# Performance work log

Hardware: AMD Instinct MI355X
Metric: run time of the kernel (lower is better)

The kernel has to match this reference:

```python
import jax, jax.numpy as jnp
import numpy as np

H = 1024      # hidden_size
NH = 4        # n_head
NP = 8        # num_points
PRED = 20     # pred_dim
FF = 4 * H    # dim_feedforward
FEATS = {"m0": 2048, "m1": 1024, "m2": 512}
B = 8192


def _ln(x, g, b, eps=1e-5):
    mu = x.mean(-1, keepdims=True)
    var = ((x - mu) ** 2).mean(-1, keepdims=True)
    return (x - mu) * jax.lax.rsqrt(var + eps) * g + b


def setup_inputs() -> dict:
    key = jax.random.key(0)
    ks = iter(jax.random.split(key, 64))
    d = {}
    d["x_m0"] = jax.random.normal(next(ks), (B, FEATS["m0"]), jnp.float32)
    d["x_m1"] = jax.random.normal(next(ks), (B, 8, FEATS["m1"]), jnp.float32)  # 3D -> mean over dim 1
    d["x_m2"] = jax.random.normal(next(ks), (B, FEATS["m2"]), jnp.float32)

    def p(shape):
        return jax.random.normal(next(ks), shape, jnp.float32) * 0.02

    # modality projectors (Linear stored as [in, out]; y = x @ W + b)
    for mm, f in FEATS.items():
        d[f"Wp_{mm}"] = p((f, H)); d[f"bp_{mm}"] = jnp.zeros((H,), jnp.float32)
    # gated fusion
    d["Wg"] = p((H * 3, 3)); d["bg"] = jnp.zeros((3,), jnp.float32)
    # deformable cross attention
    d["Woff"] = p((H, NH * NP)); d["boff"] = jnp.zeros((NH * NP,), jnp.float32)
    d["Watt"] = p((H, NH * NP)); d["batt"] = jnp.zeros((NH * NP,), jnp.float32)
    d["Wproj"] = p((H * NH, H)); d["bproj"] = jnp.zeros((H,), jnp.float32)
    # FFN + layernorms
    d["W1"] = p((H, FF)); d["b1"] = jnp.zeros((FF,), jnp.float32)
    d["W2"] = p((FF, H)); d["b2"] = jnp.zeros((H,), jnp.float32)
    d["g1"] = jnp.ones((H,), jnp.float32); d["be1"] = jnp.zeros((H,), jnp.float32)
    d["g2"] = jnp.ones((H,), jnp.float32); d["be2"] = jnp.zeros((H,), jnp.float32)
    # head
    d["Wh"] = p((H, PRED)); d["bh"] = jnp.zeros((PRED,), jnp.float32)
    return d


def reference(x_m0, x_m1, x_m2, Wp_m0, bp_m0, Wp_m1, bp_m1, Wp_m2, bp_m2,
              Wg, bg, Woff, boff, Watt, batt, Wproj, bproj,
              W1, b1, W2, b2, g1, be1, g2, be2, Wh, bh):
    # modality projection (dropout is identity in eval mode)
    r0 = jax.nn.relu(x_m0 @ Wp_m0 + bp_m0)
    r1 = jax.nn.relu(x_m1.mean(axis=1) @ Wp_m1 + bp_m1)  # mean over dim 1 for 3D input
    r2 = jax.nn.relu(x_m2 @ Wp_m2 + bp_m2)

    # gated fusion (all modalities present -> mask adds 0 everywhere)
    cat = jnp.concatenate([r0, r1, r2], axis=-1)            # [B, 3H]
    gw = jax.nn.softmax(cat @ Wg + bg, axis=-1)             # [B, 3]
    fused = jnp.einsum('bm,bmh->bh', gw, jnp.stack([r0, r1, r2], axis=1))

    src = fused[:, None, :]                                  # [B, Lq=1, H]
    Bsz, Lq, C = src.shape
    Lk = Lq

    # DeformableCrossAttention(src, src, src)
    off = jax.nn.sigmoid((src @ Woff + boff).reshape(Bsz, Lq, NH, NP)) * (Lk - 1)
    idx = jnp.clip(off.astype(jnp.int32), 0, Lk - 1)         # torch .long() truncation (non-negative)
    al = (src @ Watt + batt).reshape(Bsz, Lq, NH, NP)
    # per-batch gather of key/value rows at sampled indices; key == value == src
    sk = jax.vmap(lambda k, i: k[i])(src, idx)               # [B, Lq, NH, NP, C]
    scores = (src[:, :, None, None, :] * sk).sum(-1) / jnp.sqrt(jnp.float32(C)) + al
    w = jax.nn.softmax(scores, axis=-1)                      # softmax over points
    attn = (w[..., None] * sk).sum(axis=3).reshape(Bsz, Lq, NH * C)
    src2 = attn @ Wproj + bproj

    src = _ln(src + src2, g1, be1)
    src2 = jax.nn.gelu(src @ W1 + b1, approximate=False) @ W2 + b2
    src = _ln(src + src2, g2, be2)

    pooled = src.mean(axis=1)                                # [B, H]
    logits = pooled @ Wh + bh                                # [B, PRED]
    hazards = jax.nn.sigmoid(logits)
    survival = jnp.cumprod(1.0 - hazards, axis=1)
    return hazards, survival
```

## Files before the change

### kernel.cpp

```cpp
#include <hip/hip_runtime.h>
#include <hip/hip_bf16.h>


#define B_ROWS 8192
#define HDIM 1024
#define F0 2048
#define F1 1024
#define F2 512
#define FFDIM 4096
#define NPRED 20

typedef __bf16 bf16x8 __attribute__((ext_vector_type(8)));
typedef float f32x4 __attribute__((ext_vector_type(4)));

__device__ __forceinline__ unsigned short f2bf(float f) {
    unsigned int u = __builtin_bit_cast(unsigned int, f);
    u += 0x7FFFu + ((u >> 16) & 1u);
    return (unsigned short)(u >> 16);
}
__device__ __forceinline__ float bf2f(unsigned short s) {
    unsigned int u = ((unsigned int)s) << 16;
    return __builtin_bit_cast(float, u);
}
__device__ __forceinline__ unsigned int pack2(float lo, float hi) {
    return (unsigned int)f2bf(lo) | ((unsigned int)f2bf(hi) << 16);
}

template <int EPI>
__global__ __launch_bounds__(256) void gemm_bt(
    const unsigned short* __restrict__ A,
    const unsigned short* __restrict__ Bt,
    const float* __restrict__ bias,
    const float* __restrict__ resid,
    void* __restrict__ outp,
    int N, int K)
{
    __shared__ __attribute__((aligned(16))) unsigned short lsA[128 * 64];
    __shared__ __attribute__((aligned(16))) unsigned short lsB[128 * 64];
    const int t = threadIdx.x;
    const int lane = t & 63;
    const int wid = t >> 6;
    const int bn = blockIdx.x, bm = blockIdx.y;
    const int wr = wid >> 1, wc = wid & 1;

    f32x4 acc[4][4] = {};

    int rowj[4], scj[4];
#pragma unroll
    for (int j = 0; j < 4; ++j) {
        int o = j * 4096 + wid * 1024 + lane * 16;
        int r = o >> 7;
        int c16 = (o >> 4) & 7;
        rowj[j] = r;
        scj[j] = c16 ^ (r & 7);
    }
    const unsigned short* Abase = A + (size_t)bm * 128 * K;
    const unsigned short* Bbase = Bt + (size_t)bn * 128 * K;

    const int ktiles = K >> 6;
    for (int kt = 0; kt < ktiles; ++kt) {
        const int k0 = kt * 64;
#pragma unroll
        for (int j = 0; j < 4; ++j) {
            const unsigned short* ga = Abase + (size_t)rowj[j] * K + k0 + scj[j] * 8;
            const unsigned short* gb = Bbase + (size_t)rowj[j] * K + k0 + scj[j] * 8;
            __builtin_amdgcn_global_load_lds(
                (const __attribute__((address_space(1))) unsigned int*)ga,
                (__attribute__((address_space(3))) unsigned int*)(lsA + j * 2048 + wid * 512),
                16, 0, 0);
            __builtin_amdgcn_global_load_lds(
                (const __attribute__((address_space(1))) unsigned int*)gb,
                (__attribute__((address_space(3))) unsigned int*)(lsB + j * 2048 + wid * 512),
                16, 0, 0);
        }
        __syncthreads();
#pragma unroll
        for (int ks = 0; ks < 2; ++ks) {
            bf16x8 af[4], bfr[4];
            const int kc = ks * 4 + (lane >> 4);
#pragma unroll
            for (int m = 0; m < 4; ++m) {
                int r = wr * 64 + m * 16 + (lane & 15);
                af[m] = *(const bf16x8*)(lsA + r * 64 + ((kc ^ (r & 7)) << 3));
            }
#pragma unroll
            for (int n = 0; n < 4; ++n) {
                int r = wc * 64 + n * 16 + (lane & 15);
                bfr[n] = *(const bf16x8*)(lsB + r * 64 + ((kc ^ (r & 7)) << 3));
            }
#pragma unroll
            for (int m = 0; m < 4; ++m)
#pragma unroll
                for (int n = 0; n < 4; ++n)
                    acc[m][n] = __builtin_amdgcn_mfma_f32_16x16x32_bf16(
                        af[m], bfr[n], acc[m][n], 0, 0, 0);
        }
        __syncthreads();
    }

#pragma unroll
    for (int n = 0; n < 4; ++n) {
        const int col = bn * 128 + wc * 64 + n * 16 + (lane & 15);
        const float bv = bias[col];
#pragma unroll
        for (int m = 0; m < 4; ++m) {
            const int row0 = bm * 128 + wr * 64 + m * 16 + ((lane >> 4) << 2);
#pragma unroll
            for (int r2 = 0; r2 < 4; ++r2) {
                const size_t idx = (size_t)(row0 + r2) * N + col;
                float v = acc[m][n][r2] + bv;
                if (EPI == 0) {
                    v = v > 0.f ? v : 0.f;
                    ((unsigned short*)outp)[idx] = f2bf(v);
                } else if (EPI == 1) {
                    float g = 0.5f * v * (1.f + erff(v * 0.70710678118654752f));
                    ((unsigned short*)outp)[idx] = f2bf(g);
                } else {
                    ((float*)outp)[idx] = v + resid[idx];
                }
            }
        }
    }
}

template <int OUT_BF16>
__global__ void transpose_k(const float* __restrict__ in, void* __restrict__ out,
                            int R, int C)
{
    __shared__ float tile[32][33];
    const int r0 = blockIdx.y * 32, c0 = blockIdx.x * 32;
    const int tx = threadIdx.x, ty = threadIdx.y;
#pragma unroll
    for (int i = 0; i < 4; ++i) {
        int r = r0 + ty + i * 8, c = c0 + tx;
        if (r < R && c < C) tile[ty + i * 8][tx] = in[(size_t)r * C + c];
    }
    __syncthreads();
#pragma unroll
    for (int i = 0; i < 4; ++i) {
        int c = c0 + ty + i * 8, r = r0 + tx;
        if (r < R && c < C) {
            float v = tile[tx][ty + i * 8];
            if (OUT_BF16) ((unsigned short*)out)[(size_t)c * R + r] = f2bf(v);
            else          ((float*)out)[(size_t)c * R + r] = v;
        }
    }
}

__global__ void wproj_sum_k(const float* __restrict__ Wproj,
                            unsigned short* __restrict__ WPT)
{
    __shared__ float tile[32][33];
    const int k0 = blockIdx.y * 32, n0 = blockIdx.x * 32;
    const int tx = threadIdx.x, ty = threadIdx.y;
#pragma unroll
    for (int i = 0; i < 4; ++i) {
        int k = k0 + ty + i * 8, n = n0 + tx;
        float s = 0.f;
#pragma unroll
        for (int h = 0; h < 4; ++h) s += Wproj[(size_t)(h * HDIM + k) * HDIM + n];
        tile[ty + i * 8][tx] = s;
    }
    __syncthreads();
#pragma unroll
    for (int i = 0; i < 4; ++i) {
        int n = n0 + ty + i * 8, k = k0 + tx;
        WPT[(size_t)n * HDIM + k] = f2bf(tile[tx][ty + i * 8]);
    }
}

__global__ void cvt_f32_bf16_k(const float* __restrict__ in,
                               unsigned short* __restrict__ out, int n8)
{
    for (int i = blockIdx.x * blockDim.x + threadIdx.x; i < n8;
         i += gridDim.x * blockDim.x) {
        const float4* p = (const float4*)(in + (size_t)i * 8);
        float4 a = p[0], b = p[1];
        uint4 o;
        o.x = pack2(a.x, a.y); o.y = pack2(a.z, a.w);
        o.z = pack2(b.x, b.y); o.w = pack2(b.z, b.w);
        *(uint4*)(out + (size_t)i * 8) = o;
    }
}

__global__ void mean8_k(const float* __restrict__ x, unsigned short* __restrict__ out,
                        int nq)
{
    for (int q = blockIdx.x * blockDim.x + threadIdx.x; q < nq;
         q += gridDim.x * blockDim.x) {
        int b = q >> 8, c4 = (q & 255) << 2;
        const float* base = x + (size_t)b * 8 * HDIM + c4;
        float4 s = {0.f, 0.f, 0.f, 0.f};
#pragma unroll
        for (int s8 = 0; s8 < 8; ++s8) {
            float4 v = *(const float4*)(base + s8 * HDIM);
            s.x += v.x; s.y += v.y; s.z += v.z; s.w += v.w;
        }
        uint2 o;
        o.x = pack2(s.x * 0.125f, s.y * 0.125f);
        o.y = pack2(s.z * 0.125f, s.w * 0.125f);
        *(uint2*)(out + (size_t)b * HDIM + c4) = o;
    }
}

__global__ __launch_bounds__(256) void gating_k(
    const unsigned short* __restrict__ r0p, const unsigned short* __restrict__ r1p,
    const unsigned short* __restrict__ r2p,
    const float* __restrict__ WgT,
    const float* __restrict__ bg,
    unsigned short* __restrict__ fusedb, float* __restrict__ fusedf)
{
    const int row = blockIdx.x * 4 + (threadIdx.x >> 6);
    const int lane = threadIdx.x & 63;
    float rv[3][16];
    const unsigned short* rp[3] = {r0p, r1p, r2p};
#pragma unroll
    for (int m = 0; m < 3; ++m) {
        const uint4* p = (const uint4*)(rp[m] + (size_t)row * HDIM + lane * 16);
        uint4 u0 = p[0], u1 = p[1];
        unsigned int w[8] = {u0.x, u0.y, u0.z, u0.w, u1.x, u1.y, u1.z, u1.w};
#pragma unroll
        for (int q = 0; q < 8; ++q) {
            rv[m][q * 2]     = bf2f((unsigned short)(w[q] & 0xffffu));
            rv[m][q * 2 + 1] = bf2f((unsigned short)(w[q] >> 16));
        }
    }
    float s[3] = {0.f, 0.f, 0.f};
#pragma unroll
    for (int j = 0; j < 3; ++j) {
#pragma unroll
        for (int m = 0; m < 3; ++m) {
            const float* wp = WgT + j * 3072 + m * HDIM + lane * 16;
#pragma unroll
            for (int e = 0; e < 16; ++e) s[j] += rv[m][e] * wp[e];
        }
    }
#pragma unroll
    for (int j = 0; j < 3; ++j)
#pragma unroll
        for (int off = 32; off > 0; off >>= 1) s[j] += __shfl_xor(s[j], off);

    float s0 = s[0] + bg[0], s1 = s[1] + bg[1], s2 = s[2] + bg[2];
    float mx = fmaxf(s0, fmaxf(s1, s2));
    float e0 = expf(s0 - mx), e1 = expf(s1 - mx), e2 = expf(s2 - mx);
    float inv = 1.f / (e0 + e1 + e2);
    float g0 = e0 * inv, g1 = e1 * inv, g2 = e2 * inv;

    float f[16];
#pragma unroll
    for (int e = 0; e < 16; ++e)
        f[e] = g0 * rv[0][e] + g1 * rv[1][e] + g2 * rv[2][e];

    float4* ff = (float4*)(fusedf + (size_t)row * HDIM + lane * 16);
#pragma unroll
    for (int q = 0; q < 4; ++q) {
        float4 v = {f[q * 4], f[q * 4 + 1], f[q * 4 + 2], f[q * 4 + 3]};
        ff[q] = v;
    }
    uint4* fb = (uint4*)(fusedb + (size_t)row * HDIM + lane * 16);
    uint4 o0, o1;
    o0.x = pack2(f[0], f[1]);  o0.y = pack2(f[2], f[3]);
    o0.z = pack2(f[4], f[5]);  o0.w = pack2(f[6], f[7]);
    o1.x = pack2(f[8], f[9]);  o1.y = pack2(f[10], f[11]);
    o1.z = pack2(f[12], f[13]); o1.w = pack2(f[14], f[15]);
    fb[0] = o0; fb[1] = o1;
}

__global__ __launch_bounds__(256) void ln_k(
    const float* __restrict__ z, const float* __restrict__ g,
    const float* __restrict__ be,
    unsigned short* __restrict__ yb, float* __restrict__ yf)
{
    const int row = blockIdx.x * 4 + (threadIdx.x >> 6);
    const int lane = threadIdx.x & 63;
    const float4* zp = (const float4*)(z + (size_t)row * HDIM + lane * 16);
    float x[16];
    float4 v0 = zp[0], v1 = zp[1], v2 = zp[2], v3 = zp[3];
    x[0]=v0.x; x[1]=v0.y; x[2]=v0.z; x[3]=v0.w;
    x[4]=v1.x; x[5]=v1.y; x[6]=v1.z; x[7]=v1.w;
    x[8]=v2.x; x[9]=v2.y; x[10]=v2.z; x[11]=v2.w;
    x[12]=v3.x; x[13]=v3.y; x[14]=v3.z; x[15]=v3.w;
    float sum = 0.f, sq = 0.f;
#pragma unroll
    for (int e = 0; e < 16; ++e) { sum += x[e]; sq += x[e] * x[e]; }
#pragma unroll
    for (int off = 32; off > 0; off >>= 1) {
        sum += __shfl_xor(sum, off);
        sq  += __shfl_xor(sq, off);
    }
    float mu = sum * (1.f / HDIM);
    float var = sq * (1.f / HDIM) - mu * mu;
    float rs = rsqrtf(var + 1e-5f);
    const float4* gp = (const float4*)(g + lane * 16);
    const float4* bp = (const float4*)(be + lane * 16);
    float y[16];
#pragma unroll
    for (int q = 0; q < 4; ++q) {
        float4 gv = gp[q], bv = bp[q];
        y[q*4+0] = (x[q*4+0] - mu) * rs * gv.x + bv.x;
        y[q*4+1] = (x[q*4+1] - mu) * rs * gv.y + bv.y;
        y[q*4+2] = (x[q*4+2] - mu) * rs * gv.z + bv.z;
        y[q*4+3] = (x[q*4+3] - mu) * rs * gv.w + bv.w;
    }
    float4* yfp = (float4*)(yf + (size_t)row * HDIM + lane * 16);
#pragma unroll
    for (int q = 0; q < 4; ++q) {
        float4 v = {y[q*4], y[q*4+1], y[q*4+2], y[q*4+3]};
        yfp[q] = v;
    }
    uint4* ybp = (uint4*)(yb + (size_t)row * HDIM + lane * 16);
    uint4 o0, o1;
    o0.x = pack2(y[0], y[1]);   o0.y = pack2(y[2], y[3]);
    o0.z = pack2(y[4], y[5]);   o0.w = pack2(y[6], y[7]);
    o1.x = pack2(y[8], y[9]);   o1.y = pack2(y[10], y[11]);
    o1.z = pack2(y[12], y[13]); o1.w = pack2(y[14], y[15]);
    ybp[0] = o0; ybp[1] = o1;
}

__global__ __launch_bounds__(256) void head_k(
    const float* __restrict__ z, const float* __restrict__ g,
    const float* __restrict__ be,
    const float* __restrict__ WhT,
    const float* __restrict__ bh, float* __restrict__ out)
{
    const int row = blockIdx.x * 4 + (threadIdx.x >> 6);
    const int lane = threadIdx.x & 63;
    const float4* zp = (const float4*)(z + (size_t)row * HDIM + lane * 16);
    float x[16];
    float4 v0 = zp[0], v1 = zp[1], v2 = zp[2], v3 = zp[3];
    x[0]=v0.x; x[1]=v0.y; x[2]=v0.z; x[3]=v0.w;
    x[4]=v1.x; x[5]=v1.y; x[6]=v1.z; x[7]=v1.w;
    x[8]=v2.x; x[9]=v2.y; x[10]=v2.z; x[11]=v2.w;
    x[12]=v3.x; x[13]=v3.y; x[14]=v3.z; x[15]=v3.w;
    float sum = 0.f, sq = 0.f;
#pragma unroll
    for (int e = 0; e < 16; ++e) { sum += x[e]; sq += x[e] * x[e]; }
#pragma unroll
    for (int off = 32; off > 0; off >>= 1) {
        sum += __shfl_xor(sum, off);
        sq  += __shfl_xor(sq, off);
    }
    float mu = sum * (1.f / HDIM);
    float var = sq * (1.f / HDIM) - mu * mu;
    float rs = rsqrtf(var + 1e-5f);
    const float4* gp = (const float4*)(g + lane * 16);
    const float4* bp = (const float4*)(be + lane * 16);
    float h[16];
#pragma unroll
    for (int q = 0; q < 4; ++q) {
        float4 gv = gp[q], bv = bp[q];
        h[q*4+0] = (x[q*4+0] - mu) * rs * gv.x + bv.x;
        h[q*4+1] = (x[q*4+1] - mu) * rs * gv.y + bv.y;
        h[q*4+2] = (x[q*4+2] - mu) * rs * gv.z + bv.z;
        h[q*4+3] = (x[q*4+3] - mu) * rs * gv.w + bv.w;
    }
    float lg[NPRED];
#pragma unroll
    for (int j = 0; j < NPRED; ++j) {
        const float4* wp = (const float4*)(WhT + j * HDIM + lane * 16);
        float4 w0 = wp[0], w1 = wp[1], w2 = wp[2], w3 = wp[3];
        float d = h[0]*w0.x + h[1]*w0.y + h[2]*w0.z + h[3]*w0.w
                + h[4]*w1.x + h[5]*w1.y + h[6]*w1.z + h[7]*w1.w
                + h[8]*w2.x + h[9]*w2.y + h[10]*w2.z + h[11]*w2.w
                + h[12]*w3.x + h[13]*w3.y + h[14]*w3.z + h[15]*w3.w;
#pragma unroll
        for (int off = 32; off > 0; off >>= 1) d += __shfl_xor(d, off);
        lg[j] = d;
    }
    if (lane == 0) {
        float sv = 1.f;
#pragma unroll
        for (int j = 0; j < NPRED; ++j) {
            float l = lg[j] + bh[j];
            float hz = 1.f / (1.f + expf(-l));
            sv *= (1.f - hz);
            out[(size_t)row * NPRED + j] = hz;
            out[(size_t)B_ROWS * NPRED + (size_t)row * NPRED + j] = sv;
        }
    }
}

constexpr size_t SZ_XB0   = (size_t)B_ROWS * F0 * 2;
constexpr size_t SZ_XB1M  = (size_t)B_ROWS * HDIM * 2;
constexpr size_t SZ_XB2   = (size_t)B_ROWS * F2 * 2;
constexpr size_t SZ_R     = (size_t)B_ROWS * HDIM * 2;
constexpr size_t SZ_F32H  = (size_t)B_ROWS * HDIM * 4;

constexpr size_t OFF_XB0   = 0;
constexpr size_t OFF_XB1M  = OFF_XB0 + SZ_XB0;
constexpr size_t OFF_XB2   = OFF_XB1M + SZ_XB1M;
constexpr size_t OFF_R0    = OFF_XB2 + SZ_XB2;
constexpr size_t OFF_R1    = OFF_R0 + SZ_R;
constexpr size_t OFF_R2    = OFF_R1 + SZ_R;
constexpr size_t OFF_FUSEB = OFF_R2 + SZ_R;
constexpr size_t OFF_FUSEF = OFF_FUSEB + SZ_R;
constexpr size_t OFF_Z2    = OFF_FUSEF + SZ_F32H;
constexpr size_t OFF_WT0   = OFF_Z2 + SZ_F32H;
constexpr size_t OFF_WT1   = OFF_WT0 + (size_t)HDIM * F0 * 2;
constexpr size_t OFF_WT2   = OFF_WT1 + (size_t)HDIM * F1 * 2;
constexpr size_t OFF_WPT   = OFF_WT2 + (size_t)HDIM * F2 * 2;
constexpr size_t OFF_W1T   = OFF_WPT + (size_t)HDIM * HDIM * 2;
constexpr size_t OFF_W2T   = OFF_W1T + (size_t)FFDIM * HDIM * 2;
constexpr size_t OFF_WGT   = OFF_W2T + (size_t)HDIM * FFDIM * 2;
constexpr size_t OFF_WHT   = OFF_WGT + (size_t)3 * 3072 * 4;
constexpr size_t OFF_Z1   = OFF_XB0;
constexpr size_t OFF_H1B  = OFF_XB1M;
constexpr size_t OFF_H1F  = OFF_R0;
constexpr size_t OFF_HMID = OFF_R2;

static inline void launch_gemm(int epi, const void* A, const void* Bt,
                               const float* bias, const float* resid, void* outp,
                               int M, int N, int K, hipStream_t s)
{
    dim3 grid(N / 128, M / 128), blk(256);
    if (epi == 0)
        gemm_bt<0><<<grid, blk, 0, s>>>((const unsigned short*)A,
            (const unsigned short*)Bt, bias, resid, outp, N, K);
    else if (epi == 1)
        gemm_bt<1><<<grid, blk, 0, s>>>((const unsigned short*)A,
            (const unsigned short*)Bt, bias, resid, outp, N, K);
    else
        gemm_bt<2><<<grid, blk, 0, s>>>((const unsigned short*)A,
            (const unsigned short*)Bt, bias, resid, outp, N, K);
}

extern "C" void kernel_launch(void* const* d_in, const int* in_sizes, int n_in,
                              void* d_out, int out_size, void* d_ws, size_t ws_size,
                              hipStream_t stream)
{
    const float* x_m0  = (const float*)d_in[0];
    const float* x_m1  = (const float*)d_in[1];
    const float* x_m2  = (const float*)d_in[2];
    const float* Wp_m0 = (const float*)d_in[3];
    const float* bp_m0 = (const float*)d_in[4];
    const float* Wp_m1 = (const float*)d_in[5];
    const float* bp_m1 = (const float*)d_in[6];
    const float* Wp_m2 = (const float*)d_in[7];
    const float* bp_m2 = (const float*)d_in[8];
    const float* Wg    = (const float*)d_in[9];
    const float* bg    = (const float*)d_in[10];
    const float* Wproj = (const float*)d_in[15];
    const float* bproj = (const float*)d_in[16];
    const float* W1    = (const float*)d_in[17];
    const float* b1    = (const float*)d_in[18];
    const float* W2    = (const float*)d_in[19];
    const float* b2    = (const float*)d_in[20];
    const float* g1    = (const float*)d_in[21];
    const float* be1   = (const float*)d_in[22];
    const float* g2    = (const float*)d_in[23];
    const float* be2   = (const float*)d_in[24];
    const float* Wh    = (const float*)d_in[25];
    const float* bh    = (const float*)d_in[26];

    char* ws = (char*)d_ws;
    unsigned short* xb0   = (unsigned short*)(ws + OFF_XB0);
    unsigned short* xb1m  = (unsigned short*)(ws + OFF_XB1M);
    unsigned short* xb2   = (unsigned short*)(ws + OFF_XB2);
    unsigned short* r0    = (unsigned short*)(ws + OFF_R0);
    unsigned short* r1    = (unsigned short*)(ws + OFF_R1);
    unsigned short* r2    = (unsigned short*)(ws + OFF_R2);
    unsigned short* fuseb = (unsigned short*)(ws + OFF_FUSEB);
    float*          fusef = (float*)(ws + OFF_FUSEF);
    float*          z2    = (float*)(ws + OFF_Z2);
    unsigned short* WT0   = (unsigned short*)(ws + OFF_WT0);
    unsigned short* WT1   = (unsigned short*)(ws + OFF_WT1);
    unsigned short* WT2   = (unsigned short*)(ws + OFF_WT2);
    unsigned short* WPT   = (unsigned short*)(ws + OFF_WPT);
    unsigned short* W1T   = (unsigned short*)(ws + OFF_W1T);
    unsigned short* W2T   = (unsigned short*)(ws + OFF_W2T);
    float*          WgT   = (float*)(ws + OFF_WGT);
    float*          WhT   = (float*)(ws + OFF_WHT);
    float*          z1    = (float*)(ws + OFF_Z1);
    unsigned short* h1b   = (unsigned short*)(ws + OFF_H1B);
    float*          h1f   = (float*)(ws + OFF_H1F);
    unsigned short* hmid  = (unsigned short*)(ws + OFF_HMID);
    float*          outp  = (float*)d_out;

    dim3 tb(32, 8);
    transpose_k<1><<<dim3(HDIM/32, F0/32), tb, 0, stream>>>(Wp_m0, WT0, F0, HDIM);
    transpose_k<1><<<dim3(HDIM/32, F1/32), tb, 0, stream>>>(Wp_m1, WT1, F1, HDIM);
    transpose_k<1><<<dim3(HDIM/32, F2/32), tb, 0, stream>>>(Wp_m2, WT2, F2, HDIM);
    transpose_k<1><<<dim3(FFDIM/32, HDIM/32), tb, 0, stream>>>(W1, W1T, HDIM, FFDIM);
    transpose_k<1><<<dim3(HDIM/32, FFDIM/32), tb, 0, stream>>>(W2, W2T, FFDIM, HDIM);
    transpose_k<0><<<dim3(1, 3072/32), tb, 0, stream>>>(Wg, WgT, 3072, 3);
    transpose_k<0><<<dim3(1, HDIM/32), tb, 0, stream>>>(Wh, WhT, HDIM, NPRED);
    wproj_sum_k<<<dim3(HDIM/32, HDIM/32), tb, 0, stream>>>(Wproj, WPT);

    cvt_f32_bf16_k<<<2048, 256, 0, stream>>>(x_m0, xb0, B_ROWS * F0 / 8);
    cvt_f32_bf16_k<<<2048, 256, 0, stream>>>(x_m2, xb2, B_ROWS * F2 / 8);
    mean8_k<<<2048, 256, 0, stream>>>(x_m1, xb1m, B_ROWS * 256);

    launch_gemm(0, xb0,  WT0, bp_m0, nullptr, r0, B_ROWS, HDIM, F0, stream);
    launch_gemm(0, xb1m, WT1, bp_m1, nullptr, r1, B_ROWS, HDIM, F1, stream);
    launch_gemm(0, xb2,  WT2, bp_m2, nullptr, r2, B_ROWS, HDIM, F2, stream);

    gating_k<<<B_ROWS / 4, 256, 0, stream>>>(r0, r1, r2, WgT, bg, fuseb, fusef);

    launch_gemm(2, fuseb, WPT, bproj, fusef, z1, B_ROWS, HDIM, HDIM, stream);

    ln_k<<<B_ROWS / 4, 256, 0, stream>>>(z1, g1, be1, h1b, h1f);

    launch_gemm(1, h1b, W1T, b1, nullptr, hmid, B_ROWS, FFDIM, HDIM, stream);
    launch_gemm(2, hmid, W2T, b2, h1f, z2, B_ROWS, HDIM, FFDIM, stream);

    head_k<<<B_ROWS / 4, 256, 0, stream>>>(z2, g2, be2, WhT, bh, outp);
}
```

Measured before the change: 983.9 us.

## Double-buffer LDS tiles in bf16 GEMM to overlap global loads with MFMA

Adds a second LDS buffer for the A and B tiles and prefetches the next K-tile via global_load_lds while the current tile is consumed by MFMAs. One of the two barriers per K-iteration is removed. This doubles shared memory per block, which may reduce occupancy, and the remaining barrier still waits on outstanding loads.

```diff
diff --git a/kernel.cpp b/kernel.cpp
--- a/kernel.cpp
+++ b/kernel.cpp
@@ -35,8 +35,8 @@
     void* __restrict__ outp,
     int N, int K)
 {
-    __shared__ __attribute__((aligned(16))) unsigned short lsA[128 * 64];
-    __shared__ __attribute__((aligned(16))) unsigned short lsB[128 * 64];
+    __shared__ __attribute__((aligned(16))) unsigned short lsA[2][128 * 64];
+    __shared__ __attribute__((aligned(16))) unsigned short lsB[2][128 * 64];
     const int t = threadIdx.x;
     const int lane = t & 63;
     const int wid = t >> 6;
@@ -58,22 +58,46 @@
     const unsigned short* Bbase = Bt + (size_t)bn * 128 * K;
 
     const int ktiles = K >> 6;
-    for (int kt = 0; kt < ktiles; ++kt) {
-        const int k0 = kt * 64;
+
+    {
+        const int k0 = 0;
 #pragma unroll
         for (int j = 0; j < 4; ++j) {
             const unsigned short* ga = Abase + (size_t)rowj[j] * K + k0 + scj[j] * 8;
             const unsigned short* gb = Bbase + (size_t)rowj[j] * K + k0 + scj[j] * 8;
             __builtin_amdgcn_global_load_lds(
                 (const __attribute__((address_space(1))) unsigned int*)ga,
-                (__attribute__((address_space(3))) unsigned int*)(lsA + j * 2048 + wid * 512),
+                (__attribute__((address_space(3))) unsigned int*)(&lsA[0][0] + j * 2048 + wid * 512),
                 16, 0, 0);
             __builtin_amdgcn_global_load_lds(
                 (const __attribute__((address_space(1))) unsigned int*)gb,
-                (__attribute__((address_space(3))) unsigned int*)(lsB + j * 2048 + wid * 512),
+                (__attribute__((address_space(3))) unsigned int*)(&lsB[0][0] + j * 2048 + wid * 512),
                 16, 0, 0);
         }
         __syncthreads();
+    }
+
+    int cur = 0;
+    for (int kt = 0; kt < ktiles; ++kt) {
+        if (kt + 1 < ktiles) {
+            const int k0 = (kt + 1) * 64;
+            const int nb = cur ^ 1;
+#pragma unroll
+            for (int j = 0; j < 4; ++j) {
+                const unsigned short* ga = Abase + (size_t)rowj[j] * K + k0 + scj[j] * 8;
+                const unsigned short* gb = Bbase + (size_t)rowj[j] * K + k0 + scj[j] * 8;
+                __builtin_amdgcn_global_load_lds(
+                    (const __attribute__((address_space(1))) unsigned int*)ga,
+                    (__attribute__((address_space(3))) unsigned int*)(&lsA[nb][0] + j * 2048 + wid * 512),
+                    16, 0, 0);
+                __builtin_amdgcn_global_load_lds(
+                    (const __attribute__((address_space(1))) unsigned int*)gb,
+                    (__attribute__((address_space(3))) unsigned int*)(&lsB[nb][0] + j * 2048 + wid * 512),
+                    16, 0, 0);
+            }
+        }
+        const unsigned short* la = &lsA[cur][0];
+        const unsigned short* lb = &lsB[cur][0];
 #pragma unroll
         for (int ks = 0; ks < 2; ++ks) {
             bf16x8 af[4], bfr[4];
@@ -81,12 +105,12 @@
 #pragma unroll
             for (int m = 0; m < 4; ++m) {
                 int r = wr * 64 + m * 16 + (lane & 15);
-                af[m] = *(const bf16x8*)(lsA + r * 64 + ((kc ^ (r & 7)) << 3));
+                af[m] = *(const bf16x8*)(la + r * 64 + ((kc ^ (r & 7)) << 3));
             }
 #pragma unroll
             for (int n = 0; n < 4; ++n) {
                 int r = wc * 64 + n * 16 + (lane & 15);
-                bfr[n] = *(const bf16x8*)(lsB + r * 64 + ((kc ^ (r & 7)) << 3));
+                bfr[n] = *(const bf16x8*)(lb + r * 64 + ((kc ^ (r & 7)) << 3));
             }
 #pragma unroll
             for (int m = 0; m < 4; ++m)
@@ -95,7 +119,8 @@
                     acc[m][n] = __builtin_amdgcn_mfma_f32_16x16x32_bf16(
                         af[m], bfr[n], acc[m][n], 0, 0, 0);
         }
-        __syncthreads();
+        if (kt + 1 < ktiles) __syncthreads();
+        cur ^= 1;
     }
 
 #pragma unroll
```

Result: no change. 984.5 us (+0.1%).
